# Kernel optimization log

Measured on AMD Instinct MI355X. Metric: run time of the kernel, lower is better.

The kernel has to match this reference:

```python
import jax, jax.numpy as jnp
import numpy as np

B, LS, LT = 64, 64, 64
E, H = 512, 512
VS, VT = 32000, 32000


def setup_inputs() -> dict:
    key = jax.random.key(0)
    ks = jax.random.split(key, 16)
    s = 0.02
    inp = {
        "src": jax.random.randint(ks[0], (B, LS), 0, VS),
        "tgt": jax.random.randint(ks[1], (B, LT), 0, VT),
        # encoder params
        "src_embed": jax.random.normal(ks[2], (VS, E), jnp.float32) * s,
        "enc_Wx": jax.random.normal(ks[3], (E, 4 * H), jnp.float32) * s,   # [i|f|g|o]
        "enc_Wh": jax.random.normal(ks[4], (H, 4 * H), jnp.float32) * s,
        "enc_b": jnp.zeros((4 * H,), jnp.float32),
        # decoder params
        "tgt_embed": jax.random.normal(ks[5], (VT, E), jnp.float32) * s,
        "att_Wh": jax.random.normal(ks[6], (H, H), jnp.float32) * s,
        "att_Ws": jax.random.normal(ks[7], (H, H), jnp.float32) * s,
        "att_v": jax.random.normal(ks[8], (H,), jnp.float32) * s,
        "dec_Wx": jax.random.normal(ks[9], (E + H, 4 * H), jnp.float32) * s,
        "dec_Wh": jax.random.normal(ks[10], (H, 4 * H), jnp.float32) * s,
        "dec_b": jnp.zeros((4 * H,), jnp.float32),
        "h2o_W": jax.random.normal(ks[11], (2 * H, VT), jnp.float32) * s,
        "h2o_b": jnp.zeros((VT,), jnp.float32),
    }
    return inp


def _lstm_step(x, h, c, Wx, Wh, b):
    # x:(B,in), h,c:(B,H). Gates packed as [i|f|g|o] along last dim (same math
    # as 8 separate nn.Linear calls with biases summed).
    z = x @ Wx + h @ Wh + b
    i, f, g, o = jnp.split(z, 4, axis=-1)
    c_new = jax.nn.sigmoid(f) * c + jax.nn.sigmoid(i) * jnp.tanh(g)
    h_new = jax.nn.sigmoid(o) * jnp.tanh(c_new)
    return h_new, c_new


def reference(src, tgt, src_embed, enc_Wx, enc_Wh, enc_b, tgt_embed,
              att_Wh, att_Ws, att_v, dec_Wx, dec_Wh, dec_b, h2o_W, h2o_b):
    Bs = src.shape[0]
    h0 = jnp.zeros((Bs, H), jnp.float32)
    c0 = jnp.zeros((Bs, H), jnp.float32)

    # ---- encoder: scan over source timesteps ----
    src_emb = src_embed[src]                       # (B,Ls,E)
    xs_enc = jnp.swapaxes(src_emb, 0, 1)           # (Ls,B,E)

    def enc_step(carry, x):
        h, c = carry
        h, c = _lstm_step(x, h, c, enc_Wx, enc_Wh, enc_b)
        return (h, c), h

    (h_enc, c_enc), enc_hs = jax.lax.scan(enc_step, (h0, c0), xs_enc)
    enc_hiddens = jnp.swapaxes(enc_hs, 0, 1)       # (B,Ls,H)

    # encoder-side attention projection is decoder-state independent: hoist it
    enc_t = enc_hiddens @ att_Wh                   # (B,Ls,H)

    # ---- decoder: teacher forcing, scan over target timesteps ----
    tgt_emb = tgt_embed[tgt]                       # (B,Lt,E)
    xs_dec = jnp.swapaxes(tgt_emb, 0, 1)           # (Lt,B,E)

    def dec_step(carry, emb):
        h, c = carry
        # Bahdanau additive attention on previous decoder hidden h
        dec_t = h @ att_Ws                                        # (B,H)
        energy = jnp.tanh(enc_t + dec_t[:, None, :]) @ att_v      # (B,Ls)
        attn = jax.nn.softmax(energy, axis=-1)                    # (B,Ls)
        context = jnp.einsum('bs,bsh->bh', attn, enc_hiddens)     # (B,H)
        lstm_in = jnp.concatenate([emb, context], axis=-1)        # (B,E+H)
        h, c = _lstm_step(lstm_in, h, c, dec_Wx, dec_Wh, dec_b)
        logits = jnp.concatenate([h, context], axis=-1) @ h2o_W + h2o_b
        out = jax.nn.log_softmax(logits, axis=-1)                 # (B,Vt)
        return (h, c), out

    _, outs = jax.lax.scan(dec_step, (h_enc, c_enc), xs_dec)      # (Lt,B,Vt)
    return jnp.swapaxes(outs, 0, 1)                               # (B,Lt,Vt)
```

## Files before the change

kernel.cpp:

```cpp
#include <hip/hip_runtime.h>
#include <hip/hip_bf16.h>
#include <math.h>

#define BB 64
#define LL 64
#define EE 512
#define HH 512
#define G4 2048
#define VT 32000
#define RT 4096

typedef unsigned short u16;
typedef unsigned int u32;
typedef unsigned char u8;
typedef __attribute__((ext_vector_type(2))) unsigned int u32x2;
typedef __attribute__((ext_vector_type(8))) unsigned short ushort8;
typedef __attribute__((ext_vector_type(8))) short bf16x8;
typedef __attribute__((ext_vector_type(4))) float f32x4;

__device__ u16   gW2T[(size_t)VT * 1024];
__device__ u16   gEncWxT[G4 * EE];
__device__ u16   gEncWhT[G4 * HH];
__device__ u16   gAttWhT[HH * HH];
__device__ u16   gDecWxTe[G4 * EE];
__device__ u16   gDecWxTc[G4 * HH];
__device__ u16   gDecWhT[G4 * HH];
__device__ u8    gWs8[HH * HH];
__device__ u16   gSrcEmb[RT * EE];
__device__ u16   gTgtEmb[RT * EE];
__device__ float gXWxE[(size_t)RT * G4];
__device__ float gXWxD[(size_t)RT * G4];
__device__ u16   gEncHb[(size_t)RT * HH];
__device__ u16   gEncHb2[(size_t)RT * HH];
__device__ u16   gEncTb[(size_t)RT * HH];
__device__ u16   gHcat[(size_t)RT * 1024];
__device__ float gC[BB * HH];
__device__ float gAv[HH];
__device__ unsigned gFlagE[64];
__device__ unsigned gFlagB[64];
__device__ unsigned gFlagC[64];
__device__ unsigned gStep;

__device__ __forceinline__ u16 f2b(float f) {
    union { float f; unsigned u; } v{f};
    unsigned r = v.u + 0x7fffu + ((v.u >> 16) & 1u);
    return (u16)(r >> 16);
}
__device__ __forceinline__ float b2f(u16 x) {
    union { unsigned u; float f; } v; v.u = ((unsigned)x) << 16; return v.f;
}
__device__ __forceinline__ float sigm(float x) { return 1.f / (1.f + __expf(-x)); }
__device__ __forceinline__ float ftanh(float x) {
    x = fminf(15.f, fmaxf(-15.f, x));
    float e = __expf(2.f * x);
    return (e - 1.f) / (e + 1.f);
}

__device__ unsigned char encf8(float f) {
    union { float f; unsigned u; } v{f};
    unsigned s = (v.u >> 31) << 7;
    float af = fabsf(f);
    if (af < 0.0009765625f) return (unsigned char)s;
    if (af >= 448.f) return (unsigned char)(s | 0x7E);
    if (af < 0.015625f) {
        int q = (int)rintf(af * 512.f);
        if (q >= 8) return (unsigned char)(s | 0x08);
        return (unsigned char)(s | q);
    }
    int e; float m = frexpf(af, &e);
    int E = e - 1 + 7;
    int q = (int)rintf((m * 2.f - 1.f) * 8.f);
    if (q == 8) { E++; q = 0; }
    if (E >= 15) return (unsigned char)(s | 0x7E);
    return (unsigned char)(s | (E << 3) | q);
}
__device__ __forceinline__ float decf8s(unsigned v) {
    unsigned s = v >> 7, e = (v >> 3) & 15, m = v & 7;
    float mag = e ? ldexpf((float)(8 + m), (int)e - 10) : ldexpf((float)m, -9);
    return s ? -mag : mag;
}
#if __has_builtin(__builtin_amdgcn_cvt_f32_fp8)
#define DEC8(w, sel) __builtin_amdgcn_cvt_f32_fp8((int)(w), sel)
#else
#define DEC8(w, sel) decf8s(((w) >> (8 * (sel))) & 0xFFu)
#endif

__device__ __forceinline__ void ld16(const void* addr, bf16x8* a) {
    asm volatile(
        "global_load_dwordx4 %0, %16, off sc0 sc1\n\t"
        "global_load_dwordx4 %1, %16, off offset:64 sc0 sc1\n\t"
        "global_load_dwordx4 %2, %16, off offset:128 sc0 sc1\n\t"
        "global_load_dwordx4 %3, %16, off offset:192 sc0 sc1\n\t"
        "global_load_dwordx4 %4, %16, off offset:256 sc0 sc1\n\t"
        "global_load_dwordx4 %5, %16, off offset:320 sc0 sc1\n\t"
        "global_load_dwordx4 %6, %16, off offset:384 sc0 sc1\n\t"
        "global_load_dwordx4 %7, %16, off offset:448 sc0 sc1\n\t"
        "global_load_dwordx4 %8, %16, off offset:512 sc0 sc1\n\t"
        "global_load_dwordx4 %9, %16, off offset:576 sc0 sc1\n\t"
        "global_load_dwordx4 %10, %16, off offset:640 sc0 sc1\n\t"
        "global_load_dwordx4 %11, %16, off offset:704 sc0 sc1\n\t"
        "global_load_dwordx4 %12, %16, off offset:768 sc0 sc1\n\t"
        "global_load_dwordx4 %13, %16, off offset:832 sc0 sc1\n\t"
        "global_load_dwordx4 %14, %16, off offset:896 sc0 sc1\n\t"
        "global_load_dwordx4 %15, %16, off offset:960 sc0 sc1\n\t"
        "s_waitcnt vmcnt(0)"
        : "=&v"(a[0]), "=&v"(a[1]), "=&v"(a[2]), "=&v"(a[3]),
          "=&v"(a[4]), "=&v"(a[5]), "=&v"(a[6]), "=&v"(a[7]),
          "=&v"(a[8]), "=&v"(a[9]), "=&v"(a[10]), "=&v"(a[11]),
          "=&v"(a[12]), "=&v"(a[13]), "=&v"(a[14]), "=&v"(a[15])
        : "v"(addr) : "memory");
}
__device__ __forceinline__ u32 ld1(const void* addr) {
    u32 r;
    asm volatile("global_load_dword %0, %1, off sc0 sc1\n\ts_waitcnt vmcnt(0)"
                 : "=&v"(r) : "v"(addr) : "memory");
    return r;
}
__device__ __forceinline__ void st8b(void* p, u32x2 v) {
    asm volatile("global_store_dwordx2 %0, %1, off sc0 sc1" :: "v"(p), "v"(v) : "memory");
}
__device__ __forceinline__ void st32b(u32* p, u32 v) {
    asm volatile("global_store_dword %0, %1, off sc0 sc1" :: "v"(p), "v"(v) : "memory");
}

__device__ __forceinline__ void setflag(unsigned* f, unsigned v) {
    asm volatile("s_waitcnt vmcnt(0)" ::: "memory");
    __syncthreads();
    if (threadIdx.x == 0) st32b((u32*)f, v);
}
__device__ __forceinline__ void waitflags(unsigned* flags, int n, unsigned target) {
    if (threadIdx.x < 64) {
        const unsigned* p = flags + (threadIdx.x & (n - 1));
        for (;;) {
            u32 v = ld1(p);
            if (__all(v >= target)) break;
            __builtin_amdgcn_s_sleep(1);
        }
    }
    __syncthreads();
}

__device__ __forceinline__ void g2l16(const u16* g, u16* l) {
    __builtin_amdgcn_global_load_lds(
        (const __attribute__((address_space(1))) unsigned int*)g,
        (__attribute__((address_space(3))) unsigned int*)l, 16, 0, 0);
}
__device__ __forceinline__ void g2l16nt(const u16* g, u16* l) {
    __builtin_amdgcn_global_load_lds(
        (const __attribute__((address_space(1))) unsigned int*)g,
        (__attribute__((address_space(3))) unsigned int*)l, 16, 0, 2);
}

__device__ inline u16* bf16sel(int s) {
    switch (s) {
        case 0: return gW2T;    case 1: return gEncWxT; case 2: return gEncWhT;
        case 3: return gAttWhT; case 4: return gDecWxTe; case 5: return gDecWxTc;
        default: return gDecWhT;
    }
}

__global__ __launch_bounds__(256) void k_transpose(const float* __restrict__ in, int R, int C, int sel) {
    __shared__ float tile[32][33];
    int tx = threadIdx.x & 31, ty0 = threadIdx.x >> 5;
    int c0 = blockIdx.x * 32, r0 = blockIdx.y * 32;
#pragma unroll
    for (int k = 0; k < 4; k++) {
        int ty = ty0 + k * 8;
        tile[ty][tx] = in[(size_t)(r0 + ty) * C + c0 + tx];
    }
    __syncthreads();
    u16* out = bf16sel(sel);
#pragma unroll
    for (int k = 0; k < 4; k++) {
        int ty = ty0 + k * 8;
        out[(size_t)(c0 + ty) * R + r0 + tx] = f2b(tile[tx][ty]);
    }
}

__global__ __launch_bounds__(256) void k_tofp8(const float* __restrict__ in) {
    int i = blockIdx.x * 256 + threadIdx.x;
    gWs8[i] = encf8(in[i]);
}

__global__ __launch_bounds__(256) void k_gather(const int* __restrict__ tok, const float* __restrict__ tab, int sel) {
    int r = blockIdx.x;
    int b = r & 63, t = r >> 6;
    int token = tok[b * LL + t];
    u16* dst = (sel == 0) ? gSrcEmb : gTgtEmb;
    const float* srow = tab + (size_t)token * EE;
    for (int e = threadIdx.x; e < EE; e += 256)
        dst[(size_t)r * EE + e] = f2b(srow[e]);
}

__global__ __launch_bounds__(256) void k_zero() {
    int i = blockIdx.x * 256 + threadIdx.x;
    gC[i] = 0.f;
    if (i < 64) st32b((u32*)(gFlagE + i), 0u);
}

__global__ __launch_bounds__(256) void k_rst(const float* __restrict__ av) {
    int t = threadIdx.x;
    gAv[t] = av[t];
    gAv[t + 256] = av[t + 256];
    if (t < 64) {
        st32b((u32*)(gFlagB + t), 0u);
        st32b((u32*)(gFlagC + t), 0u);
    }
    if (t == 0) st32b((u32*)&gStep, 0u);
}

__global__ __launch_bounds__(256) void k_gemm(int selA, int lda, int selB, int ldb,
                                              int M, int N, int K, int epi,
                                              const float* __restrict__ bias, int selOut) {
    __shared__ u16 sA[128 * 72];
    __shared__ u16 sB[128 * 72];
    const u16* Ag;
    switch (selA) { case 0: Ag = gSrcEmb; break; case 1: Ag = gTgtEmb; break; default: Ag = gEncHb; }
    const u16* Bg;
    switch (selB) { case 0: Bg = gEncWxT; break; case 1: Bg = gDecWxTe; break; default: Bg = gAttWhT; }
    float* Cg = (selOut == 0) ? gXWxE : gXWxD;

    int tid = threadIdx.x, l = tid & 63, wid = tid >> 6, wr = wid >> 1, wc = wid & 1;
    int ar = l & 15, ak = (l >> 4) * 8;
    int rowM = blockIdx.y * 128, colN = blockIdx.x * 128;
    f32x4 acc[4][4];
#pragma unroll
    for (int m = 0; m < 4; m++)
#pragma unroll
        for (int n = 0; n < 4; n++) acc[m][n] = (f32x4){0.f, 0.f, 0.f, 0.f};

    for (int k0 = 0; k0 < K; k0 += 64) {
#pragma unroll
        for (int it = 0; it < 4; it++) {
            int idx = it * 256 + tid;
            int row = idx >> 3, cc = idx & 7;
            *(ushort8*)(sA + row * 72 + cc * 8) =
                *(const ushort8*)(Ag + (size_t)(rowM + row) * lda + k0 + cc * 8);
            *(ushort8*)(sB + row * 72 + cc * 8) =
                *(const ushort8*)(Bg + (size_t)(colN + row) * ldb + k0 + cc * 8);
        }
        __syncthreads();
#pragma unroll
        for (int ks = 0; ks < 2; ks++) {
            bf16x8 a[4], b[4];
#pragma unroll
            for (int m = 0; m < 4; m++) a[m] = *(const bf16x8*)(sA + (wr * 64 + m * 16 + ar) * 72 + ks * 32 + ak);
#pragma unroll
            for (int n = 0; n < 4; n++) b[n] = *(const bf16x8*)(sB + (wc * 64 + n * 16 + ar) * 72 + ks * 32 + ak);
#pragma unroll
            for (int m = 0; m < 4; m++)
#pragma unroll
                for (int n = 0; n < 4; n++)
                    acc[m][n] = __builtin_amdgcn_mfma_f32_16x16x32_bf16(a[m], b[n], acc[m][n], 0, 0, 0);
        }
        __syncthreads();
    }
    int rb = (l >> 4) * 4;
#pragma unroll
    for (int m = 0; m < 4; m++)
#pragma unroll
        for (int n = 0; n < 4; n++)
#pragma unroll
            for (int ri = 0; ri < 4; ri++) {
                int row = rowM + wr * 64 + m * 16 + rb + ri;
                int col = colN + wc * 64 + n * 16 + ar;
                float v = acc[m][n][ri];
                if (epi == 2) Cg[(size_t)row * N + col] = v + bias[col];
                else gEncTb[(size_t)((row & 63) * 64 + (row >> 6)) * N + col] = f2b(v);
            }
}

__global__ __launch_bounds__(256) void k_encoder(int dummy) {
    __shared__ u16 sW[64 * 512];
    __shared__ u16 s_hout[64 * 16];
    int tid = threadIdx.x, l = tid & 63, wid = tid >> 6;
    int j = blockIdx.x;
#pragma unroll
    for (int it = 0; it < 16; it++) {
        int idx = it * 256 + tid;
        int lr = idx >> 6, kc = idx & 63;
        int gcol = (lr >> 4) * 512 + j * 16 + (lr & 15);
        int off = (lr * 1024 + kc * 16) ^ ((lr & 7) << 4);
        *(ushort8*)((char*)sW + off) = *(const ushort8*)(gEncWhT + (size_t)gcol * 512 + kc * 8);
    }
    __syncthreads();
    int ar = l & 15, ak = (l >> 4) * 8, rb = (l >> 4) * 4;
    int arow = wid * 16 + ar, aoff = (l >> 4) * 16;
    int hcol = j * 16 + ar;
    for (int t = 0; t < LL; t++) {
        float xwv[4][4];
#pragma unroll
        for (int ri = 0; ri < 4; ri++) {
            const float* xw = gXWxE + (size_t)(t * BB + wid * 16 + rb + ri) * G4;
#pragma unroll
            for (int g = 0; g < 4; g++) xwv[ri][g] = xw[g * 512 + hcol];
        }
        f32x4 acc[4];
#pragma unroll
        for (int g = 0; g < 4; g++) acc[g] = (f32x4){0.f, 0.f, 0.f, 0.f};
        if (t > 0) {
            waitflags(gFlagE, 32, (unsigned)t);
            bf16x8 af[16];
            ld16((const char*)gEncHb + (size_t)((t - 1) * BB + arow) * 1024 + aoff, af);
#pragma unroll
            for (int kk = 0; kk < 16; kk++) {
                int k = kk * 32 + ak;
#pragma unroll
                for (int g = 0; g < 4; g++) {
                    int lr = g * 16 + ar;
                    bf16x8 b = *(const bf16x8*)((char*)sW + ((lr * 1024 + k * 2) ^ ((lr & 7) << 4)));
                    acc[g] = __builtin_amdgcn_mfma_f32_16x16x32_bf16(af[kk], b, acc[g], 0, 0, 0);
                }
            }
        }
#pragma unroll
        for (int ri = 0; ri < 4; ri++) {
            int row = wid * 16 + rb + ri;
            float zi = acc[0][ri] + xwv[ri][0];
            float zf = acc[1][ri] + xwv[ri][1];
            float zg = acc[2][ri] + xwv[ri][2];
            float zo = acc[3][ri] + xwv[ri][3];
            float co = gC[row * HH + hcol];
            float cn = sigm(zf) * co + sigm(zi) * ftanh(zg);
            float hn = sigm(zo) * ftanh(cn);
            gC[row * HH + hcol] = cn;
            s_hout[row * 16 + ar] = f2b(hn);
        }
        __syncthreads();
        {
            int row = tid >> 2, seg = tid & 3;
            u32x2 v = *(const u32x2*)(s_hout + row * 16 + seg * 4);
            st8b(gEncHb + (size_t)(t * BB + row) * HH + j * 16 + seg * 4, v);
            *(u32x2*)(gEncHb2 + (size_t)(row * LL + t) * HH + j * 16 + seg * 4) = v;
        }
        setflag(gFlagE + j, (unsigned)(t + 1));
    }
}

__global__ __launch_bounds__(256) void k_decoder(const float* __restrict__ h2o_b,
                                                 float* __restrict__ out) {
    __shared__ u16 sWh[64 * 512];
    __shared__ u16 sWx[64 * 512];
    __shared__ u16 s_hout[64 * 16];
    __shared__ float s_h[512];
    __shared__ float s_dt[512];
    __shared__ float s_av[512];
    __shared__ float s_att[64];
    __shared__ float s_red[256];
    __shared__ float s_mv[4][520];
    int tid = threadIdx.x, l = tid & 63, wid = tid >> 6;
    int bx = blockIdx.x;
    int ar = l & 15, ak = (l >> 4) * 8, rb = (l >> 4) * 4;
    int arow = wid * 16 + ar, aoff = (l >> 4) * 16;
    if (bx >= 96) {
        u16* csA = sWh;
        u16* csB = sWh + 128 * 64;
        int wr = wid >> 1, wc = wid & 1;
        int srow = wid * 32 + (l >> 3);
        int scol = (l & 7) * 8;
        int ci = bx - 96;
        for (int jt = 0; jt < 50; jt++) {
            int T = ci + 160 * jt;
            int byy = T / 250, bxx = T % 250;
            unsigned tgt = (unsigned)(2 * byy + 2);
            if (tid == 0) {
                while (ld1(&gStep) < tgt) __builtin_amdgcn_s_sleep(32);
            }
            __syncthreads();
            int rowM = byy * 128, colN = bxx * 128;
            f32x4 acc[4][4];
#pragma unroll
            for (int m = 0; m < 4; m++)
#pragma unroll
                for (int n = 0; n < 4; n++) acc[m][n] = (f32x4){0.f, 0.f, 0.f, 0.f};
            for (int k0 = 0; k0 < 1024; k0 += 64) {
#pragma unroll
                for (int c = 0; c < 4; c++) {
                    int r = srow + c * 8;
                    g2l16(gHcat + (size_t)(rowM + r) * 1024 + k0 + scol, csA + r * 64 + scol);
                    g2l16nt(gW2T + (size_t)(colN + r) * 1024 + k0 + scol, csB + r * 64 + scol);
                }
                __syncthreads();
#pragma unroll
                for (int ks = 0; ks < 2; ks++) {
                    bf16x8 a[4], b[4];
#pragma unroll
                    for (int m = 0; m < 4; m++) a[m] = *(const bf16x8*)(csA + (wr * 64 + m * 16 + ar) * 64 + ks * 32 + ak);
#pragma unroll
                    for (int n = 0; n < 4; n++) b[n] = *(const bf16x8*)(csB + (wc * 64 + n * 16 + ar) * 64 + ks * 32 + ak);
#pragma unroll
                    for (int m = 0; m < 4; m++)
#pragma unroll
                        for (int n = 0; n < 4; n++)
                            acc[m][n] = __builtin_amdgcn_mfma_f32_16x16x32_bf16(a[m], b[n], acc[m][n], 0, 0, 0);
                }
                __syncthreads();
            }
#pragma unroll
            for (int m = 0; m < 4; m++)
#pragma unroll
                for (int n = 0; n < 4; n++)
#pragma unroll
                    for (int ri = 0; ri < 4; ri++) {
                        int row = rowM + wr * 64 + m * 16 + rb + ri;
                        int col = colN + wc * 64 + n * 16 + ar;
                        out[(size_t)((row & 63) * 64 + (row >> 6)) * VT + col] = acc[m][n][ri] + h2o_b[col];
                    }
        }
        return;
    }
    if (bx >= 64) {
        int j = bx - 64;
#pragma unroll
        for (int it = 0; it < 16; it++) {
            int idx = it * 256 + tid;
            int lr = idx >> 6, kc = idx & 63;
            int gcol = (lr >> 4) * 512 + j * 16 + (lr & 15);
            int off = (lr * 1024 + kc * 16) ^ ((lr & 7) << 4);
            *(ushort8*)((char*)sWh + off) = *(const ushort8*)(gDecWhT + (size_t)gcol * 512 + kc * 8);
            *(ushort8*)((char*)sWx + off) = *(const ushort8*)(gDecWxTc + (size_t)gcol * 512 + kc * 8);
        }
    } else {
        s_av[tid] = gAv[tid];
        s_av[tid + 256] = gAv[tid + 256];
    }
    __syncthreads();
    for (int t = 0; t < LL; t++) {
        if (bx >= 64) {
            int j = bx - 64;
            int hcol = j * 16 + ar;
            float xwv[4][4];
#pragma unroll
            for (int ri = 0; ri < 4; ri++) {
                const float* xw = gXWxD + (size_t)(t * BB + wid * 16 + rb + ri) * G4;
#pragma unroll
                for (int g = 0; g < 4; g++) xwv[ri][g] = xw[g * 512 + hcol];
            }
            if (t > 0) waitflags(gFlagC, 32, (unsigned)t);
            if (t > 0 && bx == 64 && tid == 0) st32b((u32*)&gStep, (unsigned)t);
            bf16x8 af[16];
            const char* baseA = (t == 0)
                ? ((const char*)gEncHb + (size_t)(63 * BB + arow) * 1024 + aoff)
                : ((const char*)gHcat + (size_t)((t - 1) * BB + arow) * 2048 + aoff);
            ld16(baseA, af);
            f32x4 acc[4];
#pragma unroll
            for (int g = 0; g < 4; g++) acc[g] = (f32x4){0.f, 0.f, 0.f, 0.f};
#pragma unroll
            for (int kk = 0; kk < 16; kk++) {
                int k = kk * 32 + ak;
#pragma unroll
                for (int g = 0; g < 4; g++) {
                    int lr = g * 16 + ar;
                    bf16x8 b = *(const bf16x8*)((char*)sWh + ((lr * 1024 + k * 2) ^ ((lr & 7) << 4)));
                    acc[g] = __builtin_amdgcn_mfma_f32_16x16x32_bf16(af[kk], b, acc[g], 0, 0, 0);
                }
            }
            waitflags(gFlagB, 64, (unsigned)(t + 1));
            bf16x8 cf[16];
            ld16((const char*)gHcat + (size_t)(t * BB + arow) * 2048 + 1024 + aoff, cf);
#pragma unroll
            for (int kk = 0; kk < 16; kk++) {
                int k = kk * 32 + ak;
#pragma unroll
                for (int g = 0; g < 4; g++) {
                    int lr = g * 16 + ar;
                    bf16x8 b = *(const bf16x8*)((char*)sWx + ((lr * 1024 + k * 2) ^ ((lr & 7) << 4)));
                    acc[g] = __builtin_amdgcn_mfma_f32_16x16x32_bf16(cf[kk], b, acc[g], 0, 0, 0);
                }
            }
#pragma unroll
            for (int ri = 0; ri < 4; ri++) {
                int row = wid * 16 + rb + ri;
                float zi = acc[0][ri] + xwv[ri][0];
                float zf = acc[1][ri] + xwv[ri][1];
                float zg = acc[2][ri] + xwv[ri][2];
                float zo = acc[3][ri] + xwv[ri][3];
                float co = gC[row * HH + hcol];
                float cn = sigm(zf) * co + sigm(zi) * ftanh(zg);
                float hn = sigm(zo) * ftanh(cn);
                gC[row * HH + hcol] = cn;
                s_hout[row * 16 + ar] = f2b(hn);
            }
            __syncthreads();
            {
                int row = tid >> 2, seg = tid & 3;
                u32x2 v = *(const u32x2*)(s_hout + row * 16 + seg * 4);
                st8b(gHcat + (size_t)(t * BB + row) * 1024 + j * 16 + seg * 4, v);
            }
            setflag(gFlagC + j, (unsigned)(t + 1));
        } else {
            int b = bx;
            if (t > 0) waitflags(gFlagC, 32, (unsigned)t);
            const char* hb = (t == 0) ? ((const char*)gEncHb + (size_t)(63 * BB + b) * 1024)
                                      : ((const char*)gHcat + (size_t)((t - 1) * BB + b) * 2048);
            u32 hw = ld1(hb + 4 * tid);
            s_h[2 * tid] = b2f((u16)(hw & 0xffff));
            s_h[2 * tid + 1] = b2f((u16)(hw >> 16));
            __syncthreads();
            {
                int c8 = tid & 63, kq = tid >> 6;
                float a8[8];
#pragma unroll
                for (int jj = 0; jj < 8; jj++) a8[jj] = 0.f;
                const u8* wp = gWs8 + (size_t)(kq * 128) * 512 + c8 * 8;
#pragma unroll 4
                for (int i = 0; i < 128; i++) {
                    u32x2 w = *(const u32x2*)(wp + (size_t)i * 512);
                    float hk = s_h[kq * 128 + i];
                    a8[0] += hk * DEC8(w.x, 0);
                    a8[1] += hk * DEC8(w.x, 1);
                    a8[2] += hk * DEC8(w.x, 2);
                    a8[3] += hk * DEC8(w.x, 3);
                    a8[4] += hk * DEC8(w.y, 0);
                    a8[5] += hk * DEC8(w.y, 1);
                    a8[6] += hk * DEC8(w.y, 2);
                    a8[7] += hk * DEC8(w.y, 3);
                }
#pragma unroll
                for (int jj = 0; jj < 8; jj++) s_mv[kq][c8 * 8 + jj] = a8[jj];
            }
            __syncthreads();
            s_dt[tid] = s_mv[0][tid] + s_mv[1][tid] + s_mv[2][tid] + s_mv[3][tid];
            s_dt[tid + 256] = s_mv[0][tid + 256] + s_mv[1][tid + 256] + s_mv[2][tid + 256] + s_mv[3][tid + 256];
            __syncthreads();
            {
                int s = tid >> 2, q = tid & 3;
                const u16* et = gEncTb + (size_t)(b * 64 + s) * 512 + q * 128;
                const float* dtp = s_dt + q * 128;
                const float* avp = s_av + q * 128;
                float p = 0.f;
#pragma unroll
                for (int i = 0; i < 16; i++) {
                    ushort8 ev = *(const ushort8*)(et + i * 8);
#pragma unroll
                    for (int jj = 0; jj < 8; jj++) {
                        int h = i * 8 + jj;
                        p += ftanh(b2f((u16)ev[jj]) + dtp[h]) * avp[h];
                    }
                }
                s_red[tid] = p;
            }
            __syncthreads();
            if (tid < 64) {
                float v = s_red[tid * 4] + s_red[tid * 4 + 1] + s_red[tid * 4 + 2] + s_red[tid * 4 + 3];
                float m = v;
                for (int o = 32; o; o >>= 1) m = fmaxf(m, __shfl_xor(m, o));
                float e = __expf(v - m);
                float ss = e;
                for (int o = 32; o; o >>= 1) ss += __shfl_xor(ss, o);
                s_att[tid] = e / ss;
            }
            __syncthreads();
            int c = tid * 2;
            float c0 = 0.f, c1 = 0.f;
            const u16* eh = gEncHb2 + (size_t)b * LL * HH;
#pragma unroll 8
            for (int s2 = 0; s2 < 64; s2++) {
                float a = s_att[s2];
                u32 w = *(const u32*)(eh + (size_t)s2 * HH + c);
                c0 += a * b2f((u16)(w & 0xffff));
                c1 += a * b2f((u16)(w >> 16));
            }
            u32 cw = (u32)f2b(c0) | ((u32)f2b(c1) << 16);
            st32b((u32*)(gHcat + (size_t)(t * BB + b) * 1024 + 512 + c), cw);
            setflag(gFlagB + b, (unsigned)(t + 1));
        }
    }
    if (bx == 64) {
        waitflags(gFlagC, 32, 64u);
        waitflags(gFlagB, 64, 64u);
        if (tid == 0) st32b((u32*)&gStep, 64u);
    }
}

__global__ __launch_bounds__(256) void k_lsm(float* __restrict__ out) {
    int row = blockIdx.x, tid = threadIdx.x;
    float4* p4 = (float4*)(out + (size_t)row * VT);
    float m = -1e30f, s = 0.f;
    for (int i = tid; i < VT / 4; i += 256) {
        float4 v = p4[i];
        float mx = fmaxf(fmaxf(v.x, v.y), fmaxf(v.z, v.w));
        float mn = fmaxf(m, mx);
        s = s * __expf(m - mn) + __expf(v.x - mn) + __expf(v.y - mn) + __expf(v.z - mn) + __expf(v.w - mn);
        m = mn;
    }
    for (int o = 32; o; o >>= 1) {
        float m2 = __shfl_xor(m, o), s2 = __shfl_xor(s, o);
        float mn = fmaxf(m, m2);
        s = s * __expf(m - mn) + s2 * __expf(m2 - mn);
        m = mn;
    }
    __shared__ float rm[4], rs[4];
    if ((tid & 63) == 0) { rm[tid >> 6] = m; rs[tid >> 6] = s; }
    __syncthreads();
    float mm = fmaxf(fmaxf(rm[0], rm[1]), fmaxf(rm[2], rm[3]));
    float ss = rs[0] * __expf(rm[0] - mm) + rs[1] * __expf(rm[1] - mm) +
               rs[2] * __expf(rm[2] - mm) + rs[3] * __expf(rm[3] - mm);
    float lse = mm + __logf(ss);
    for (int i = tid; i < VT / 4; i += 256) {
        float4 v = p4[i];
        v.x -= lse; v.y -= lse; v.z -= lse; v.w -= lse;
        p4[i] = v;
    }
}

extern "C" void kernel_launch(void* const* d_in, const int* in_sizes, int n_in,
                              void* d_out, int out_size, void* d_ws, size_t ws_size,
                              hipStream_t stream) {
    const int*   src       = (const int*)d_in[0];
    const int*   tgt       = (const int*)d_in[1];
    const float* src_embed = (const float*)d_in[2];
    const float* enc_Wx    = (const float*)d_in[3];
    const float* enc_Wh    = (const float*)d_in[4];
    const float* enc_b     = (const float*)d_in[5];
    const float* tgt_embed = (const float*)d_in[6];
    const float* att_Wh    = (const float*)d_in[7];
    const float* att_Ws    = (const float*)d_in[8];
    const float* att_v     = (const float*)d_in[9];
    const float* dec_Wx    = (const float*)d_in[10];
    const float* dec_Wh    = (const float*)d_in[11];
    const float* dec_b     = (const float*)d_in[12];
    const float* h2o_W     = (const float*)d_in[13];
    const float* h2o_b     = (const float*)d_in[14];
    float* out = (float*)d_out;
    dim3 blk(256);

    k_transpose<<<dim3(VT / 32, 1024 / 32), blk, 0, stream>>>(h2o_W, 1024, VT, 0);
    k_transpose<<<dim3(G4 / 32, EE / 32), blk, 0, stream>>>(enc_Wx, EE, G4, 1);
    k_transpose<<<dim3(G4 / 32, HH / 32), blk, 0, stream>>>(enc_Wh, HH, G4, 2);
    k_transpose<<<dim3(HH / 32, HH / 32), blk, 0, stream>>>(att_Wh, HH, HH, 3);
    k_transpose<<<dim3(G4 / 32, EE / 32), blk, 0, stream>>>(dec_Wx, EE, G4, 4);
    k_transpose<<<dim3(G4 / 32, HH / 32), blk, 0, stream>>>(dec_Wx + (size_t)512 * G4, HH, G4, 5);
    k_transpose<<<dim3(G4 / 32, HH / 32), blk, 0, stream>>>(dec_Wh, HH, G4, 6);
    k_tofp8<<<HH * HH / 256, blk, 0, stream>>>(att_Ws);
    k_gather<<<RT, blk, 0, stream>>>(src, src_embed, 0);
    k_gather<<<RT, blk, 0, stream>>>(tgt, tgt_embed, 1);
    k_zero<<<128, blk, 0, stream>>>();
    k_gemm<<<dim3(G4 / 128, RT / 128), blk, 0, stream>>>(0, 512, 0, 512, RT, G4, 512, 2, enc_b, 0);
    k_gemm<<<dim3(G4 / 128, RT / 128), blk, 0, stream>>>(1, 512, 1, 512, RT, G4, 512, 2, dec_b, 1);
    int dummy = 0;
    void* eargs[] = { &dummy };
    hipLaunchCooperativeKernel((const void*)k_encoder, dim3(32), dim3(256), eargs, 0, stream);
    k_gemm<<<dim3(HH / 128, RT / 128), blk, 0, stream>>>(2, 512, 2, 512, RT, HH, 512, 4, nullptr, 2);
    k_rst<<<1, blk, 0, stream>>>(att_v);
    const float* h2ob = h2o_b;
    float* outp = out;
    void* dargs[] = { (void*)&h2ob, (void*)&outp };
    hipLaunchCooperativeKernel((const void*)k_decoder, dim3(256), dim3(256), dargs, 0, stream);
    k_lsm<<<RT, blk, 0, stream>>>(out);
}
```

Baseline: 2.812 ms.

## Overlap decoder input GEMM and h2o transpose with encoder recurrence

Extends the cooperative encoder launch from 32 to 256 blocks. The extra blocks compute the decoder input projection GEMM and the bf16 transpose of h2o_W while the 32 recurrence blocks run their serial timestep loop. This removes two standalone launches and hides their work behind the latency-bound encoder. It risks bandwidth contention slowing the encoder's critical path and requires all blocks to be co-resident.

```diff
diff --git a/kernel.cpp b/kernel.cpp
--- a/kernel.cpp
+++ b/kernel.cpp
@@ -153,7 +153,7 @@
 
 __device__ inline u16* bf16sel(int s) {
     switch (s) {
-        case 0: return gW2T;    case 1: return gEncWxT; case 2: return gEncWhT;
+        case 1: return gEncWxT; case 2: return gEncWhT;
         case 3: return gAttWhT; case 4: return gDecWxTe; case 5: return gDecWxTc;
         default: return gDecWhT;
     }
@@ -214,11 +214,9 @@
                                               const float* __restrict__ bias, int selOut) {
     __shared__ u16 sA[128 * 72];
     __shared__ u16 sB[128 * 72];
-    const u16* Ag;
-    switch (selA) { case 0: Ag = gSrcEmb; break; case 1: Ag = gTgtEmb; break; default: Ag = gEncHb; }
-    const u16* Bg;
-    switch (selB) { case 0: Bg = gEncWxT; break; case 1: Bg = gDecWxTe; break; default: Bg = gAttWhT; }
-    float* Cg = (selOut == 0) ? gXWxE : gXWxD;
+    const u16* Ag = (selA == 0) ? gSrcEmb : gEncHb;
+    const u16* Bg = (selB == 0) ? gEncWxT : gAttWhT;
+    float* Cg = gXWxE;
 
     int tid = threadIdx.x, l = tid & 63, wid = tid >> 6, wr = wid >> 1, wc = wid & 1;
     int ar = l & 15, ak = (l >> 4) * 8;
@@ -270,70 +268,145 @@
             }
 }
 
-__global__ __launch_bounds__(256) void k_encoder(int dummy) {
-    __shared__ u16 sW[64 * 512];
-    __shared__ u16 s_hout[64 * 16];
+__global__ __launch_bounds__(256) void k_encoder(const float* __restrict__ dec_b,
+                                                 const float* __restrict__ h2o_W) {
+    __shared__ char smem[67584];
     int tid = threadIdx.x, l = tid & 63, wid = tid >> 6;
-    int j = blockIdx.x;
-#pragma unroll
-    for (int it = 0; it < 16; it++) {
-        int idx = it * 256 + tid;
-        int lr = idx >> 6, kc = idx & 63;
-        int gcol = (lr >> 4) * 512 + j * 16 + (lr & 15);
-        int off = (lr * 1024 + kc * 16) ^ ((lr & 7) << 4);
-        *(ushort8*)((char*)sW + off) = *(const ushort8*)(gEncWhT + (size_t)gcol * 512 + kc * 8);
-    }
-    __syncthreads();
+    int bx = blockIdx.x;
     int ar = l & 15, ak = (l >> 4) * 8, rb = (l >> 4) * 4;
-    int arow = wid * 16 + ar, aoff = (l >> 4) * 16;
-    int hcol = j * 16 + ar;
-    for (int t = 0; t < LL; t++) {
-        float xwv[4][4];
-#pragma unroll
-        for (int ri = 0; ri < 4; ri++) {
-            const float* xw = gXWxE + (size_t)(t * BB + wid * 16 + rb + ri) * G4;
-#pragma unroll
-            for (int g = 0; g < 4; g++) xwv[ri][g] = xw[g * 512 + hcol];
-        }
-        f32x4 acc[4];
-#pragma unroll
-        for (int g = 0; g < 4; g++) acc[g] = (f32x4){0.f, 0.f, 0.f, 0.f};
-        if (t > 0) {
-            waitflags(gFlagE, 32, (unsigned)t);
-            bf16x8 af[16];
-            ld16((const char*)gEncHb + (size_t)((t - 1) * BB + arow) * 1024 + aoff, af);
-#pragma unroll
-            for (int kk = 0; kk < 16; kk++) {
-                int k = kk * 32 + ak;
-#pragma unroll
-                for (int g = 0; g < 4; g++) {
-                    int lr = g * 16 + ar;
-                    bf16x8 b = *(const bf16x8*)((char*)sW + ((lr * 1024 + k * 2) ^ ((lr & 7) << 4)));
-                    acc[g] = __builtin_amdgcn_mfma_f32_16x16x32_bf16(af[kk], b, acc[g], 0, 0, 0);
-                }
-            }
-        }
-#pragma unroll
-        for (int ri = 0; ri < 4; ri++) {
-            int row = wid * 16 + rb + ri;
-            float zi = acc[0][ri] + xwv[ri][0];
-            float zf = acc[1][ri] + xwv[ri][1];
-            float zg = acc[2][ri] + xwv[ri][2];
-            float zo = acc[3][ri] + xwv[ri][3];
-            float co = gC[row * HH + hcol];
-            float cn = sigm(zf) * co + sigm(zi) * ftanh(zg);
-            float hn = sigm(zo) * ftanh(cn);
-            gC[row * HH + hcol] = cn;
-            s_hout[row * 16 + ar] = f2b(hn);
+    if (bx < 32) {
+        u16* sW = (u16*)smem;
+        u16* s_hout = (u16*)(smem + 65536);
+        int j = bx;
+#pragma unroll
+        for (int it = 0; it < 16; it++) {
+            int idx = it * 256 + tid;
+            int lr = idx >> 6, kc = idx & 63;
+            int gcol = (lr >> 4) * 512 + j * 16 + (lr & 15);
+            int off = (lr * 1024 + kc * 16) ^ ((lr & 7) << 4);
+            *(ushort8*)((char*)sW + off) = *(const ushort8*)(gEncWhT + (size_t)gcol * 512 + kc * 8);
         }
         __syncthreads();
-        {
-            int row = tid >> 2, seg = tid & 3;
-            u32x2 v = *(const u32x2*)(s_hout + row * 16 + seg * 4);
-            st8b(gEncHb + (size_t)(t * BB + row) * HH + j * 16 + seg * 4, v);
-            *(u32x2*)(gEncHb2 + (size_t)(row * LL + t) * HH + j * 16 + seg * 4) = v;
-        }
-        setflag(gFlagE + j, (unsigned)(t + 1));
+        int arow = wid * 16 + ar, aoff = (l >> 4) * 16;
+        int hcol = j * 16 + ar;
+        for (int t = 0; t < LL; t++) {
+            float xwv[4][4];
+#pragma unroll
+            for (int ri = 0; ri < 4; ri++) {
+                const float* xw = gXWxE + (size_t)(t * BB + wid * 16 + rb + ri) * G4;
+#pragma unroll
+                for (int g = 0; g < 4; g++) xwv[ri][g] = xw[g * 512 + hcol];
+            }
+            f32x4 acc[4];
+#pragma unroll
+            for (int g = 0; g < 4; g++) acc[g] = (f32x4){0.f, 0.f, 0.f, 0.f};
+            if (t > 0) {
+                waitflags(gFlagE, 32, (unsigned)t);
+                bf16x8 af[16];
+                ld16((const char*)gEncHb + (size_t)((t - 1) * BB + arow) * 1024 + aoff, af);
+#pragma unroll
+                for (int kk = 0; kk < 16; kk++) {
+                    int k = kk * 32 + ak;
+#pragma unroll
+                    for (int g = 0; g < 4; g++) {
+                        int lr = g * 16 + ar;
+                        bf16x8 b = *(const bf16x8*)((char*)sW + ((lr * 1024 + k * 2) ^ ((lr & 7) << 4)));
+                        acc[g] = __builtin_amdgcn_mfma_f32_16x16x32_bf16(af[kk], b, acc[g], 0, 0, 0);
+                    }
+                }
+            }
+#pragma unroll
+            for (int ri = 0; ri < 4; ri++) {
+                int row = wid * 16 + rb + ri;
+                float zi = acc[0][ri] + xwv[ri][0];
+                float zf = acc[1][ri] + xwv[ri][1];
+                float zg = acc[2][ri] + xwv[ri][2];
+                float zo = acc[3][ri] + xwv[ri][3];
+                float co = gC[row * HH + hcol];
+                float cn = sigm(zf) * co + sigm(zi) * ftanh(zg);
+                float hn = sigm(zo) * ftanh(cn);
+                gC[row * HH + hcol] = cn;
+                s_hout[row * 16 + ar] = f2b(hn);
+            }
+            __syncthreads();
+            {
+                int row = tid >> 2, seg = tid & 3;
+                u32x2 v = *(const u32x2*)(s_hout + row * 16 + seg * 4);
+                st8b(gEncHb + (size_t)(t * BB + row) * HH + j * 16 + seg * 4, v);
+                *(u32x2*)(gEncHb2 + (size_t)(row * LL + t) * HH + j * 16 + seg * 4) = v;
+            }
+            setflag(gFlagE + j, (unsigned)(t + 1));
+        }
+    } else if (bx < 96) {
+        u16* sA = (u16*)smem;
+        u16* sB = (u16*)(smem + 18432);
+        int wr = wid >> 1, wc = wid & 1;
+        for (int it8 = 0; it8 < 8; it8++) {
+            int ti = (bx - 32) * 8 + it8;
+            int bxx = ti & 15, byy = ti >> 4;
+            int rowM = byy * 128, colN = bxx * 128;
+            f32x4 acc[4][4];
+#pragma unroll
+            for (int m = 0; m < 4; m++)
+#pragma unroll
+                for (int n = 0; n < 4; n++) acc[m][n] = (f32x4){0.f, 0.f, 0.f, 0.f};
+            for (int k0 = 0; k0 < 512; k0 += 64) {
+#pragma unroll
+                for (int it = 0; it < 4; it++) {
+                    int idx = it * 256 + tid;
+                    int row = idx >> 3, cc = idx & 7;
+                    *(ushort8*)(sA + row * 72 + cc * 8) =
+                        *(const ushort8*)(gTgtEmb + (size_t)(rowM + row) * 512 + k0 + cc * 8);
+                    *(ushort8*)(sB + row * 72 + cc * 8) =
+                        *(const ushort8*)(gDecWxTe + (size_t)(colN + row) * 512 + k0 + cc * 8);
+                }
+                __syncthreads();
+#pragma unroll
+                for (int ks = 0; ks < 2; ks++) {
+                    bf16x8 a[4], b[4];
+#pragma unroll
+                    for (int m = 0; m < 4; m++) a[m] = *(const bf16x8*)(sA + (wr * 64 + m * 16 + ar) * 72 + ks * 32 + ak);
+#pragma unroll
+                    for (int n = 0; n < 4; n++) b[n] = *(const bf16x8*)(sB + (wc * 64 + n * 16 + ar) * 72 + ks * 32 + ak);
+#pragma unroll
+                    for (int m = 0; m < 4; m++)
+#pragma unroll
+                        for (int n = 0; n < 4; n++)
+                            acc[m][n] = __builtin_amdgcn_mfma_f32_16x16x32_bf16(a[m], b[n], acc[m][n], 0, 0, 0);
+                }
+                __syncthreads();
+            }
+#pragma unroll
+            for (int m = 0; m < 4; m++)
+#pragma unroll
+                for (int n = 0; n < 4; n++)
+#pragma unroll
+                    for (int ri = 0; ri < 4; ri++) {
+                        int row = rowM + wr * 64 + m * 16 + rb + ri;
+                        int col = colN + wc * 64 + n * 16 + ar;
+                        gXWxD[(size_t)row * G4 + col] = acc[m][n][ri] + dec_b[col];
+                    }
+        }
+    } else {
+        float (*tile)[33] = (float(*)[33])smem;
+        int tx = tid & 31, ty0 = tid >> 5;
+        for (int k = 0; k < 200; k++) {
+            int ti = (bx - 96) * 200 + k;
+            int ct = ti % 1000, rt = ti / 1000;
+            int c0 = ct * 32, r0 = rt * 32;
+            __syncthreads();
+#pragma unroll
+            for (int kk = 0; kk < 4; kk++) {
+                int ty = ty0 + kk * 8;
+                tile[ty][tx] = h2o_W[(size_t)(r0 + ty) * VT + c0 + tx];
+            }
+            __syncthreads();
+#pragma unroll
+            for (int kk = 0; kk < 4; kk++) {
+                int ty = ty0 + kk * 8;
+                gW2T[(size_t)(c0 + ty) * 1024 + r0 + tx] = f2b(tile[tx][ty]);
+            }
+        }
     }
 }
 
@@ -626,7 +699,6 @@
     float* out = (float*)d_out;
     dim3 blk(256);
 
-    k_transpose<<<dim3(VT / 32, 1024 / 32), blk, 0, stream>>>(h2o_W, 1024, VT, 0);
     k_transpose<<<dim3(G4 / 32, EE / 32), blk, 0, stream>>>(enc_Wx, EE, G4, 1);
     k_transpose<<<dim3(G4 / 32, HH / 32), blk, 0, stream>>>(enc_Wh, HH, G4, 2);
     k_transpose<<<dim3(HH / 32, HH / 32), blk, 0, stream>>>(att_Wh, HH, HH, 3);
@@ -638,10 +710,10 @@
     k_gather<<<RT, blk, 0, stream>>>(tgt, tgt_embed, 1);
     k_zero<<<128, blk, 0, stream>>>();
     k_gemm<<<dim3(G4 / 128, RT / 128), blk, 0, stream>>>(0, 512, 0, 512, RT, G4, 512, 2, enc_b, 0);
-    k_gemm<<<dim3(G4 / 128, RT / 128), blk, 0, stream>>>(1, 512, 1, 512, RT, G4, 512, 2, dec_b, 1);
-    int dummy = 0;
-    void* eargs[] = { &dummy };
-    hipLaunchCooperativeKernel((const void*)k_encoder, dim3(32), dim3(256), eargs, 0, stream);
+    const float* decb = dec_b;
+    const float* h2ow = h2o_W;
+    void* eargs[] = { (void*)&decb, (void*)&h2ow };
+    hipLaunchCooperativeKernel((const void*)k_encoder, dim3(256), dim3(256), eargs, 0, stream);
     k_gemm<<<dim3(HH / 128, RT / 128), blk, 0, stream>>>(2, 512, 2, 512, RT, HH, 512, 4, nullptr, 2);
     k_rst<<<1, blk, 0, stream>>>(att_v);
     const float* h2ob = h2o_b;
```

Measured after the change: 2.774 ms. No clear change (-1.4%).
